# Kernel optimization log

Hardware: AMD Instinct MI355X
Metric: run time of the kernel (lower is better)

Reference implementation:

```python
import jax, jax.numpy as jnp
import numpy as np
import math

D_MODEL, D_K, D_V, N_HEADS = 1024, 64, 64, 16

def setup_inputs() -> dict:
    key = jax.random.key(0)
    ks = jax.random.split(key, 5)
    x = jax.random.normal(ks[0], (4, 2048, D_MODEL), dtype=jnp.float32)
    s = 1.0 / math.sqrt(D_MODEL)
    # per-head projection weights, stacked: [H, D, d_k] (equivalent to H separate nn.Linear(D, d_k, bias=False))
    Wq = jax.random.normal(ks[1], (N_HEADS, D_MODEL, D_K), dtype=jnp.float32) * s
    Wk = jax.random.normal(ks[2], (N_HEADS, D_MODEL, D_K), dtype=jnp.float32) * s
    Wv = jax.random.normal(ks[3], (N_HEADS, D_MODEL, D_V), dtype=jnp.float32) * s
    # output projection: Linear(d_value*n_heads, d_model, bias=False) -> [H*d_v, D]
    Wo = jax.random.normal(ks[4], (N_HEADS * D_V, D_MODEL), dtype=jnp.float32) * (1.0 / math.sqrt(N_HEADS * D_V))
    return {"x": x, "Wq": Wq, "Wk": Wk, "Wv": Wv, "Wo": Wo}

def reference(x, Wq, Wk, Wv, Wo):
    d_k = Wq.shape[-1]
    # batched per-head projections (fuses the per-head Python loop into one einsum)
    Q = jnp.einsum('bsd,hdk->bhsk', x, Wq)
    K = jnp.einsum('bsd,hdk->bhsk', x, Wk)
    V = jnp.einsum('bsd,hdv->bhsv', x, Wv)
    scores = jnp.einsum('bhqk,bhsk->bhqs', Q, K) / jnp.sqrt(jnp.asarray(d_k, x.dtype))
    weights = jax.nn.softmax(scores, axis=-1)
    heads = jnp.einsum('bhqs,bhsv->bhqv', weights, V)
    B, H, S, Dv = heads.shape
    # concat heads along last dim (head-major order, matching torch.cat of per-head outputs)
    concat = jnp.transpose(heads, (0, 2, 1, 3)).reshape(B, S, H * Dv)
    return concat @ Wo
```

## Files before the change

### kernel.cpp

```cpp
#include <hip/hip_runtime.h>


typedef __attribute__((ext_vector_type(8))) short bf16x8;
typedef __attribute__((ext_vector_type(4))) float f32x4;
typedef __attribute__((ext_vector_type(4))) unsigned short ushortx4;

__device__ __forceinline__ unsigned short f2bf(float x) {
    unsigned int u = __float_as_uint(x);
    u += 0x7FFFu + ((u >> 16) & 1u);
    return (unsigned short)(u >> 16);
}
__device__ __forceinline__ unsigned int pack_bf2(float hi, float lo) {
    return __builtin_amdgcn_perm(__float_as_uint(hi), __float_as_uint(lo), 0x07060302u);
}

__device__ __forceinline__ void gload_lds16(const unsigned short* g, unsigned short* lds) {
    __builtin_amdgcn_global_load_lds(
        (const __attribute__((address_space(1))) unsigned int*)g,
        (__attribute__((address_space(3))) unsigned int*)lds,
        16, 0, 0);
}

__global__ __launch_bounds__(256) void pack_all(
    const float* __restrict__ x,
    const float* __restrict__ Wq,
    const float* __restrict__ Wk,
    const float* __restrict__ Wv,
    const float* __restrict__ Wo,
    unsigned short* __restrict__ XB,
    unsigned short* __restrict__ WQKVT,
    unsigned short* __restrict__ WOT)
{
    const int bid = blockIdx.x;
    bf16x8 v;
    if (bid < 4096) {
        size_t base = ((size_t)bid * 256 + threadIdx.x) * 8;
        float4 f0 = *(const float4*)&x[base];
        float4 f1 = *(const float4*)&x[base + 4];
        v[0] = f2bf(f0.x); v[1] = f2bf(f0.y); v[2] = f2bf(f0.z); v[3] = f2bf(f0.w);
        v[4] = f2bf(f1.x); v[5] = f2bf(f1.y); v[6] = f2bf(f1.z); v[7] = f2bf(f1.w);
        *(bf16x8*)&XB[base] = v;
    } else if (bid < 5632) {
        int i = (bid - 4096) * 256 + threadIdx.x;
        int d0 = (i * 8) & 1023;
        int n  = (i * 8) >> 10;
        int part = n >> 10;
        int hkk  = n & 1023;
        int h = hkk >> 6, kk = hkk & 63;
        const float* W = (part == 0) ? Wq : ((part == 1) ? Wk : Wv);
        float scale = (part == 0) ? 0.125f * 1.44269504088896f : 1.0f;
        #pragma unroll
        for (int e = 0; e < 8; ++e)
            v[e] = f2bf(W[(h << 16) + ((d0 + e) << 6) + kk] * scale);
        *(bf16x8*)&WQKVT[(size_t)n * 1024 + d0] = v;
    } else {
        int i = (bid - 5632) * 256 + threadIdx.x;
        int k0 = (i * 8) & 1023;
        int n  = (i * 8) >> 10;
        #pragma unroll
        for (int e = 0; e < 8; ++e)
            v[e] = f2bf(Wo[(size_t)(k0 + e) * 1024 + n]);
        *(bf16x8*)&WOT[(size_t)n * 1024 + k0] = v;
    }
}

template<int CMODE, int BN>
__global__ __launch_bounds__(256) void gemm_bt(
    const unsigned short* __restrict__ A,
    const unsigned short* __restrict__ Bt,
    void* __restrict__ Cv,
    unsigned short* __restrict__ VT,
    int M, int N, int K, int ldc)
{
    __shared__ __align__(16) unsigned short As[128 * 32];
    __shared__ __align__(16) unsigned short Bs[BN * 32];
    const int m0 = blockIdx.y * 128;
    const int n0 = blockIdx.x * BN;
    const int tid  = threadIdx.x;
    const int w    = tid >> 6, lane = tid & 63;
    const int q4   = lane >> 4, lr  = lane & 15;
    constexpr int MI = (BN == 128) ? 4 : 2;
    const int rowBase = (BN == 128) ? (w >> 1) * 64 : w * 32;
    const int colBase = (BN == 128) ? (w & 1) * 64 : 0;

    const int ch   = tid & 3;
    const int row0 = tid >> 2;
    unsigned short* asb0 = &As[w * 512];
    unsigned short* asb1 = &As[2048 + w * 512];
    unsigned short* bsb0 = &Bs[w * 512];
    unsigned short* bsb1 = (BN == 128) ? &Bs[2048 + w * 512] : nullptr;

    f32x4 acc[MI][4] = {};

    for (int k0 = 0; k0 < K; k0 += 32) {
        __syncthreads();
        gload_lds16(&A [(size_t)(m0 + row0)      * K + k0 + ch * 8], asb0);
        gload_lds16(&A [(size_t)(m0 + row0 + 64) * K + k0 + ch * 8], asb1);
        gload_lds16(&Bt[(size_t)(n0 + row0)      * K + k0 + ch * 8], bsb0);
        if (BN == 128)
            gload_lds16(&Bt[(size_t)(n0 + row0 + 64) * K + k0 + ch * 8], bsb1);
        __syncthreads();

        bf16x8 af[MI], bfv[4];
        #pragma unroll
        for (int i = 0; i < MI; ++i)
            af[i] = *(const bf16x8*)&As[(rowBase + i * 16 + lr) * 32 + q4 * 8];
        #pragma unroll
        for (int j = 0; j < 4; ++j)
            bfv[j] = *(const bf16x8*)&Bs[(colBase + j * 16 + lr) * 32 + q4 * 8];
        #pragma unroll
        for (int i = 0; i < MI; ++i)
            #pragma unroll
            for (int j = 0; j < 4; ++j)
                acc[i][j] = __builtin_amdgcn_mfma_f32_16x16x32_bf16(af[i], bfv[j], acc[i][j], 0, 0, 0);
    }

    #pragma unroll
    for (int i = 0; i < MI; ++i) {
        const int row = m0 + rowBase + i * 16 + q4 * 4;
        #pragma unroll
        for (int j = 0; j < 4; ++j) {
            const int col = n0 + colBase + j * 16 + lr;
            if (CMODE == 0) {
                float* C = (float*)Cv;
                #pragma unroll
                for (int p = 0; p < 4; ++p)
                    C[(size_t)(row + p) * ldc + col] = acc[i][j][p];
            } else {
                if (col < 2048) {
                    unsigned short* C = (unsigned short*)Cv;
                    #pragma unroll
                    for (int p = 0; p < 4; ++p)
                        C[(size_t)(row + p) * 2048 + col] = f2bf(acc[i][j][p]);
                } else {
                    const int c2 = col - 2048;
                    const int hh = c2 >> 6, dd = c2 & 63;
                    const int bb = row >> 11, ss = row & 2047;
                    ushortx4 v;
                    #pragma unroll
                    for (int p = 0; p < 4; ++p) v[p] = f2bf(acc[i][j][p]);
                    *(ushortx4*)&VT[((size_t)(bb * 16 + hh) * 64 + dd) * 2048 + ss] = v;
                }
            }
        }
    }
}

__global__ __launch_bounds__(256, 4) void attn_flash(
    const unsigned short* __restrict__ QK,
    const unsigned short* __restrict__ VT,
    unsigned short* __restrict__ HC)
{
    const int bh  = blockIdx.x;
    const int qb  = blockIdx.y;
    const int b   = bh >> 4, h = bh & 15;
    const int tid = threadIdx.x;
    const int w   = tid >> 6, lane = tid & 63;
    const int q4  = lane >> 4, lr  = lane & 15;

    __shared__ __align__(16) unsigned short Ks [2][64 * 64];
    __shared__ __align__(16) unsigned short Vts[2][64 * 64];

    const int drow   = tid >> 3;
    const int gchunk = (tid & 7) ^ (drow & 7);
    const unsigned short* Kg = QK + (size_t)(b * 2048) * 2048 + 1024 + h * 64;
    const unsigned short* Vg = VT + (size_t)bh * 64 * 2048;
    const unsigned short* kP0 = Kg + (size_t)(drow)      * 2048 + gchunk * 8;
    const unsigned short* kP1 = Kg + (size_t)(drow + 32) * 2048 + gchunk * 8;
    const unsigned short* vP0 = Vg + (size_t)(drow)      * 2048 + gchunk * 8;
    const unsigned short* vP1 = Vg + (size_t)(drow + 32) * 2048 + gchunk * 8;
    const int ldsOff = w * 512;

    auto dma = [&](int buf, int t) {
        gload_lds16(kP0 + (size_t)t * 131072, &Ks [buf][ldsOff]);
        gload_lds16(kP1 + (size_t)t * 131072, &Ks [buf][2048 + ldsOff]);
        gload_lds16(vP0 + t * 64,             &Vts[buf][ldsOff]);
        gload_lds16(vP1 + t * 64,             &Vts[buf][2048 + ldsOff]);
    };

    dma(0, 0);

    const int qrow0 = b * 2048 + qb * 128 + w * 32;
    bf16x8 qf[2][2];
    #pragma unroll
    for (int u = 0; u < 2; ++u)
        #pragma unroll
        for (int c = 0; c < 2; ++c)
            qf[u][c] = *(const bf16x8*)&QK[(size_t)(qrow0 + u * 16 + lr) * 2048
                                           + h * 64 + c * 32 + q4 * 8];

    const int addrA = ((q4 & 1) * 32 + lr) * 4;
    const int addrB = addrA + 64;
    const bool hiSel = (q4 >= 2);
    const int lr7 = lr & 7;

    const short oneb = (short)0x3F80;
    const bf16x8 onesf = { oneb, oneb, oneb, oneb, oneb, oneb, oneb, oneb };

    f32x4 o[2][4] = {};
    f32x4 lsum[2] = {};
    int cur = 0;

    for (int t = 0; t < 32; ++t) {
        __syncthreads();
        if (t + 1 < 32) dma(cur ^ 1, t + 1);

        unsigned int pk[2][4][2];
        #pragma unroll
        for (int mt = 0; mt < 4; ++mt) {
            f32x4 st0 = {}, st1 = {};
            #pragma unroll
            for (int c = 0; c < 2; ++c) {
                const int slot = (c * 4 + q4) ^ lr7;
                bf16x8 kf = *(const bf16x8*)&Ks[cur][(mt * 16 + lr) * 64 + slot * 8];
                st0 = __builtin_amdgcn_mfma_f32_16x16x32_bf16(kf, qf[0][c], st0, 0, 0, 0);
                st1 = __builtin_amdgcn_mfma_f32_16x16x32_bf16(kf, qf[1][c], st1, 0, 0, 0);
            }
            #pragma unroll
            for (int u = 0; u < 2; ++u) {
                f32x4 sv = u ? st1 : st0;
                float e0 = __builtin_amdgcn_exp2f(sv[0]);
                float e1 = __builtin_amdgcn_exp2f(sv[1]);
                float e2 = __builtin_amdgcn_exp2f(sv[2]);
                float e3 = __builtin_amdgcn_exp2f(sv[3]);
                pk[u][mt][0] = pack_bf2(e1, e0);
                pk[u][mt][1] = pack_bf2(e3, e2);
            }
        }

        #pragma unroll
        for (int kc = 0; kc < 2; ++kc) {
            bf16x8 pb[2];
            #pragma unroll
            for (int u = 0; u < 2; ++u) {
                const int mA = 2 * kc, mB = 2 * kc + 1;
                int w0a = __builtin_amdgcn_ds_bpermute(addrA, (int)pk[u][mA][0]);
                int w0b = __builtin_amdgcn_ds_bpermute(addrA, (int)pk[u][mB][0]);
                int w1a = __builtin_amdgcn_ds_bpermute(addrA, (int)pk[u][mA][1]);
                int w1b = __builtin_amdgcn_ds_bpermute(addrA, (int)pk[u][mB][1]);
                int w2a = __builtin_amdgcn_ds_bpermute(addrB, (int)pk[u][mA][0]);
                int w2b = __builtin_amdgcn_ds_bpermute(addrB, (int)pk[u][mB][0]);
                int w3a = __builtin_amdgcn_ds_bpermute(addrB, (int)pk[u][mA][1]);
                int w3b = __builtin_amdgcn_ds_bpermute(addrB, (int)pk[u][mB][1]);
                int4 wv;
                wv.x = hiSel ? w0b : w0a;
                wv.y = hiSel ? w1b : w1a;
                wv.z = hiSel ? w2b : w2a;
                wv.w = hiSel ? w3b : w3a;
                pb[u] = *(bf16x8*)&wv;
            }
            lsum[0] = __builtin_amdgcn_mfma_f32_16x16x32_bf16(onesf, pb[0], lsum[0], 0, 0, 0);
            lsum[1] = __builtin_amdgcn_mfma_f32_16x16x32_bf16(onesf, pb[1], lsum[1], 0, 0, 0);
            #pragma unroll
            for (int jd = 0; jd < 4; ++jd) {
                const int slot = (kc * 4 + q4) ^ lr7;
                bf16x8 vf = *(const bf16x8*)&Vts[cur][(jd * 16 + lr) * 64 + slot * 8];
                o[0][jd] = __builtin_amdgcn_mfma_f32_16x16x32_bf16(vf, pb[0], o[0][jd], 0, 0, 0);
                o[1][jd] = __builtin_amdgcn_mfma_f32_16x16x32_bf16(vf, pb[1], o[1][jd], 0, 0, 0);
            }
        }
        cur ^= 1;
    }

    #pragma unroll
    for (int u = 0; u < 2; ++u) {
        const float inv = __builtin_amdgcn_rcpf(lsum[u][0]);
        const size_t rowO = (size_t)(qrow0 + u * 16 + lr);
        #pragma unroll
        for (int jd = 0; jd < 4; ++jd) {
            ushortx4 v;
            #pragma unroll
            for (int p = 0; p < 4; ++p)
                v[p] = f2bf(o[u][jd][p] * inv);
            *(ushortx4*)&HC[rowO * 1024 + h * 64 + jd * 16 + q4 * 4] = v;
        }
    }
}

extern "C" void kernel_launch(void* const* d_in, const int* in_sizes, int n_in,
                              void* d_out, int out_size, void* d_ws, size_t ws_size,
                              hipStream_t stream)
{
    const float* x  = (const float*)d_in[0];
    const float* Wq = (const float*)d_in[1];
    const float* Wk = (const float*)d_in[2];
    const float* Wv = (const float*)d_in[3];
    const float* Wo = (const float*)d_in[4];
    float* out = (float*)d_out;

    char* ws = (char*)d_ws;
    unsigned short* XB    = (unsigned short*)(ws);
    unsigned short* HC    = (unsigned short*)(ws);
    unsigned short* WQKVT = (unsigned short*)(ws + 16777216);
    unsigned short* WOT   = (unsigned short*)(ws + 23068672);
    unsigned short* QK    = (unsigned short*)(ws + 25165824);
    unsigned short* VT    = (unsigned short*)(ws + 58720256);

    pack_all<<<6144, 256, 0, stream>>>(x, Wq, Wk, Wv, Wo, XB, WQKVT, WOT);
    gemm_bt<1, 128><<<dim3(24, 64), 256, 0, stream>>>(XB, WQKVT, QK, VT, 8192, 3072, 1024, 0);
    attn_flash<<<dim3(64, 16), 256, 0, stream>>>(QK, VT, HC);
    gemm_bt<0, 64><<<dim3(16, 64), 256, 0, stream>>>(HC, WOT, out, nullptr, 8192, 1024, 1024, 1024);
}
```

Baseline: 324.1 us.

## Double query rows per attention block to reuse K/V tiles across more queries

Each attention workgroup now handles 256 query rows (64 per wave) instead of 128, halving the grid along the query dimension. Each K/V tile loaded into LDS is reused across four 16-row query fragments, which halves global K/V traffic and per-tile sync overhead. The score and PV loops are also interleaved per key chunk so only half of the packed probabilities stay live at once. The cost is more registers (occupancy hint lowered from 4 to 2) and only 512 blocks, which means fewer waves to hide latency.

```diff
diff --git a/kernel.cpp b/kernel.cpp
--- a/kernel.cpp
+++ b/kernel.cpp
@@ -146,7 +146,7 @@
     }
 }
 
-__global__ __launch_bounds__(256, 4) void attn_flash(
+__global__ __launch_bounds__(256, 2) void attn_flash(
     const unsigned short* __restrict__ QK,
     const unsigned short* __restrict__ VT,
     unsigned short* __restrict__ HC)
@@ -180,10 +180,10 @@
 
     dma(0, 0);
 
-    const int qrow0 = b * 2048 + qb * 128 + w * 32;
-    bf16x8 qf[2][2];
+    const int qrow0 = b * 2048 + qb * 256 + w * 64;
+    bf16x8 qf[4][2];
     #pragma unroll
-    for (int u = 0; u < 2; ++u)
+    for (int u = 0; u < 4; ++u)
         #pragma unroll
         for (int c = 0; c < 2; ++c)
             qf[u][c] = *(const bf16x8*)&QK[(size_t)(qrow0 + u * 16 + lr) * 2048
@@ -197,51 +197,51 @@
     const short oneb = (short)0x3F80;
     const bf16x8 onesf = { oneb, oneb, oneb, oneb, oneb, oneb, oneb, oneb };
 
-    f32x4 o[2][4] = {};
-    f32x4 lsum[2] = {};
+    f32x4 o[4][4] = {};
+    f32x4 lsum[4] = {};
     int cur = 0;
 
     for (int t = 0; t < 32; ++t) {
         __syncthreads();
         if (t + 1 < 32) dma(cur ^ 1, t + 1);
 
-        unsigned int pk[2][4][2];
-        #pragma unroll
-        for (int mt = 0; mt < 4; ++mt) {
-            f32x4 st0 = {}, st1 = {};
-            #pragma unroll
-            for (int c = 0; c < 2; ++c) {
-                const int slot = (c * 4 + q4) ^ lr7;
-                bf16x8 kf = *(const bf16x8*)&Ks[cur][(mt * 16 + lr) * 64 + slot * 8];
-                st0 = __builtin_amdgcn_mfma_f32_16x16x32_bf16(kf, qf[0][c], st0, 0, 0, 0);
-                st1 = __builtin_amdgcn_mfma_f32_16x16x32_bf16(kf, qf[1][c], st1, 0, 0, 0);
+        #pragma unroll
+        for (int kc = 0; kc < 2; ++kc) {
+            unsigned int pk[4][2][2];
+            #pragma unroll
+            for (int ml = 0; ml < 2; ++ml) {
+                const int mt = kc * 2 + ml;
+                f32x4 st[4] = {};
+                #pragma unroll
+                for (int c = 0; c < 2; ++c) {
+                    const int slot = (c * 4 + q4) ^ lr7;
+                    bf16x8 kf = *(const bf16x8*)&Ks[cur][(mt * 16 + lr) * 64 + slot * 8];
+                    #pragma unroll
+                    for (int u = 0; u < 4; ++u)
+                        st[u] = __builtin_amdgcn_mfma_f32_16x16x32_bf16(kf, qf[u][c], st[u], 0, 0, 0);
+                }
+                #pragma unroll
+                for (int u = 0; u < 4; ++u) {
+                    float e0 = __builtin_amdgcn_exp2f(st[u][0]);
+                    float e1 = __builtin_amdgcn_exp2f(st[u][1]);
+                    float e2 = __builtin_amdgcn_exp2f(st[u][2]);
+                    float e3 = __builtin_amdgcn_exp2f(st[u][3]);
+                    pk[u][ml][0] = pack_bf2(e1, e0);
+                    pk[u][ml][1] = pack_bf2(e3, e2);
+                }
             }
-            #pragma unroll
-            for (int u = 0; u < 2; ++u) {
-                f32x4 sv = u ? st1 : st0;
-                float e0 = __builtin_amdgcn_exp2f(sv[0]);
-                float e1 = __builtin_amdgcn_exp2f(sv[1]);
-                float e2 = __builtin_amdgcn_exp2f(sv[2]);
-                float e3 = __builtin_amdgcn_exp2f(sv[3]);
-                pk[u][mt][0] = pack_bf2(e1, e0);
-                pk[u][mt][1] = pack_bf2(e3, e2);
-            }
-        }
-
-        #pragma unroll
-        for (int kc = 0; kc < 2; ++kc) {
-            bf16x8 pb[2];
-            #pragma unroll
-            for (int u = 0; u < 2; ++u) {
-                const int mA = 2 * kc, mB = 2 * kc + 1;
-                int w0a = __builtin_amdgcn_ds_bpermute(addrA, (int)pk[u][mA][0]);
-                int w0b = __builtin_amdgcn_ds_bpermute(addrA, (int)pk[u][mB][0]);
-                int w1a = __builtin_amdgcn_ds_bpermute(addrA, (int)pk[u][mA][1]);
-                int w1b = __builtin_amdgcn_ds_bpermute(addrA, (int)pk[u][mB][1]);
-                int w2a = __builtin_amdgcn_ds_bpermute(addrB, (int)pk[u][mA][0]);
-                int w2b = __builtin_amdgcn_ds_bpermute(addrB, (int)pk[u][mB][0]);
-                int w3a = __builtin_amdgcn_ds_bpermute(addrB, (int)pk[u][mA][1]);
-                int w3b = __builtin_amdgcn_ds_bpermute(addrB, (int)pk[u][mB][1]);
+
+            bf16x8 pb[4];
+            #pragma unroll
+            for (int u = 0; u < 4; ++u) {
+                int w0a = __builtin_amdgcn_ds_bpermute(addrA, (int)pk[u][0][0]);
+                int w0b = __builtin_amdgcn_ds_bpermute(addrA, (int)pk[u][1][0]);
+                int w1a = __builtin_amdgcn_ds_bpermute(addrA, (int)pk[u][0][1]);
+                int w1b = __builtin_amdgcn_ds_bpermute(addrA, (int)pk[u][1][1]);
+                int w2a = __builtin_amdgcn_ds_bpermute(addrB, (int)pk[u][0][0]);
+                int w2b = __builtin_amdgcn_ds_bpermute(addrB, (int)pk[u][1][0]);
+                int w3a = __builtin_amdgcn_ds_bpermute(addrB, (int)pk[u][0][1]);
+                int w3b = __builtin_amdgcn_ds_bpermute(addrB, (int)pk[u][1][1]);
                 int4 wv;
                 wv.x = hiSel ? w0b : w0a;
                 wv.y = hiSel ? w1b : w1a;
@@ -249,21 +249,24 @@
                 wv.w = hiSel ? w3b : w3a;
                 pb[u] = *(bf16x8*)&wv;
             }
-            lsum[0] = __builtin_amdgcn_mfma_f32_16x16x32_bf16(onesf, pb[0], lsum[0], 0, 0, 0);
-            lsum[1] = __builtin_amdgcn_mfma_f32_16x16x32_bf16(onesf, pb[1], lsum[1], 0, 0, 0);
+
+            #pragma unroll
+            for (int u = 0; u < 4; ++u)
+                lsum[u] = __builtin_amdgcn_mfma_f32_16x16x32_bf16(onesf, pb[u], lsum[u], 0, 0, 0);
             #pragma unroll
             for (int jd = 0; jd < 4; ++jd) {
                 const int slot = (kc * 4 + q4) ^ lr7;
                 bf16x8 vf = *(const bf16x8*)&Vts[cur][(jd * 16 + lr) * 64 + slot * 8];
-                o[0][jd] = __builtin_amdgcn_mfma_f32_16x16x32_bf16(vf, pb[0], o[0][jd], 0, 0, 0);
-                o[1][jd] = __builtin_amdgcn_mfma_f32_16x16x32_bf16(vf, pb[1], o[1][jd], 0, 0, 0);
+                #pragma unroll
+                for (int u = 0; u < 4; ++u)
+                    o[u][jd] = __builtin_amdgcn_mfma_f32_16x16x32_bf16(vf, pb[u], o[u][jd], 0, 0, 0);
             }
         }
         cur ^= 1;
     }
 
     #pragma unroll
-    for (int u = 0; u < 2; ++u) {
+    for (int u = 0; u < 4; ++u) {
         const float inv = __builtin_amdgcn_rcpf(lsum[u][0]);
         const size_t rowO = (size_t)(qrow0 + u * 16 + lr);
         #pragma unroll
@@ -298,6 +301,6 @@
 
     pack_all<<<6144, 256, 0, stream>>>(x, Wq, Wk, Wv, Wo, XB, WQKVT, WOT);
     gemm_bt<1, 128><<<dim3(24, 64), 256, 0, stream>>>(XB, WQKVT, QK, VT, 8192, 3072, 1024, 0);
-    attn_flash<<<dim3(64, 16), 256, 0, stream>>>(QK, VT, HC);
+    attn_flash<<<dim3(64, 8), 256, 0, stream>>>(QK, VT, HC);
     gemm_bt<0, 64><<<dim3(16, 64), 256, 0, stream>>>(HC, WOT, out, nullptr, 8192, 1024, 1024, 1024);
 }
```

New measurement: 319.6 us. Within noise of the previous version (-1.4%).
